# Optimization experiments

Hardware: AMD Instinct MI355X
Metric: run time of the kernel (lower is better)

Reference implementation:

```python
import jax, jax.numpy as jnp
import numpy as np

N, C, H, W = 16, 512, 64, 64
C_BAR, C_HAT = 64, 256


def max_pool2(t):
    # t: [n, c, h, w] -> [n, c, h//2, w//2] via 2x2 max pool
    n, c, h, w = t.shape
    return t.reshape(n, c, h // 2, 2, w // 2, 2).max(axis=(3, 5))


def setup_inputs() -> dict:
    key = jax.random.key(0)
    ks = jax.random.split(key, 6)
    x = jax.random.normal(ks[0], (N, C, H, W), dtype=jnp.float32)
    # 1x1 conv weights stored as [out_channels, in_channels]
    w_theta = jax.random.normal(ks[1], (C_BAR, C), dtype=jnp.float32) * 0.02
    w_phi = jax.random.normal(ks[2], (C_BAR, C), dtype=jnp.float32) * 0.02
    w_g = jax.random.normal(ks[3], (C_HAT, C), dtype=jnp.float32) * 0.02
    w_o = jax.random.normal(ks[4], (C, C_HAT), dtype=jnp.float32) * 0.02
    # gamma initialized to zero in the module; use a small nonzero value so the
    # attention path contributes to the output (and to gradients).
    gamma = jnp.full((1,), 0.1, dtype=jnp.float32)
    return {"x": x, "w_theta": w_theta, "w_phi": w_phi, "w_g": w_g,
            "w_o": w_o, "gamma": gamma}


def reference(x, w_theta, w_phi, w_g, w_o, gamma):
    n, c, h, w = x.shape
    hw, hw4 = h * w, (h * w) // 4
    # 1x1 conv projections (pure channel GEMMs)
    g_x = jnp.einsum('nchw,oc->nohw', x, w_g)          # [n, c_hat, h, w]
    g_x = max_pool2(g_x).reshape(n, -1, hw4)            # [n, c_hat, hw/4]
    phi_x = jnp.einsum('nchw,oc->nohw', x, w_phi)       # [n, c_bar, h, w]
    phi_x = max_pool2(phi_x).reshape(n, -1, hw4)        # [n, c_bar, hw/4]
    theta_x = jnp.einsum('nchw,oc->nohw', x, w_theta).reshape(n, -1, hw)  # [n, c_bar, hw]
    # bmm -> softmax -> bmm
    scores = jnp.einsum('nds,ndt->nst', theta_x, phi_x)  # [n, hw, hw/4]
    attn = jax.nn.softmax(scores, axis=-1)
    y = jnp.einsum('ndt,nst->nds', g_x, attn)            # [n, c_hat, hw]
    y = y.reshape(n, -1, h, w)
    o = jnp.einsum('nchw,oc->nohw', y, w_o)              # [n, c, h, w]
    return gamma[0] * o + x
```

## Files before the change

kernel.cpp:

```cpp
#include <hip/hip_runtime.h>
#include <stdint.h>

typedef unsigned short u16;
typedef u16   us4 __attribute__((ext_vector_type(4)));
typedef u16   us8 __attribute__((ext_vector_type(8)));
typedef __bf16 bf8 __attribute__((ext_vector_type(8)));
typedef float f4  __attribute__((ext_vector_type(4)));

__device__ __forceinline__ u16 f2bf(float f) {
    uint32_t u = __builtin_bit_cast(uint32_t, f);
    uint32_t r = (u + 0x7fffu + ((u >> 16) & 1u)) >> 16;
    return (u16)r;
}
__device__ __forceinline__ float bf2f(u16 s) {
    uint32_t u = ((uint32_t)s) << 16;
    return __builtin_bit_cast(float, u);
}
__device__ __forceinline__ f4 mfma16(bf8 a, bf8 b, f4 c) {
    return __builtin_amdgcn_mfma_f32_16x16x32_bf16(a, b, c, 0, 0, 0);
}
__device__ __forceinline__ u16 max4bf(u16 a, u16 b, u16 c, u16 d) {
    float m = fmaxf(fmaxf(bf2f(a), bf2f(b)), fmaxf(bf2f(c), bf2f(d)));
    return f2bf(m);
}

__global__ __launch_bounds__(256) void xt_kernel(
    const float* __restrict__ x, u16* __restrict__ Xt)
{
    const int s0 = blockIdx.x * 64, c0 = blockIdx.y * 64, n = blockIdx.z;
    const int tid = threadIdx.x;
    __shared__ u16 lds[64 * 72];

    {
        int c_loc = tid & 63, s_seg = (tid >> 6) * 16;
        const float* src = x + ((size_t)n * 512 + c0 + c_loc) * 4096 + s0 + s_seg;
        for (int i4 = 0; i4 < 4; i4++) {
            float4 f = *(const float4*)(src + i4 * 4);
            int s = s_seg + i4 * 4;
            lds[(s + 0) * 72 + c_loc] = f2bf(f.x);
            lds[(s + 1) * 72 + c_loc] = f2bf(f.y);
            lds[(s + 2) * 72 + c_loc] = f2bf(f.z);
            lds[(s + 3) * 72 + c_loc] = f2bf(f.w);
        }
    }
    __syncthreads();
    {
        int s_loc = tid >> 2, c_seg = (tid & 3) * 16;
        u16* dst = Xt + ((size_t)n * 4096 + s0 + s_loc) * 512 + c0 + c_seg;
        *(us8*)(dst)     = *(const us8*)&lds[s_loc * 72 + c_seg];
        *(us8*)(dst + 8) = *(const us8*)&lds[s_loc * 72 + c_seg + 8];
    }
}

__global__ __launch_bounds__(256) void wconv_kernel(
    const float* __restrict__ w_theta, const float* __restrict__ w_phi,
    const float* __restrict__ w_g, const float* __restrict__ w_o,
    u16* __restrict__ Wall_bf, u16* __restrict__ Wo_bf)
{
    int base = (blockIdx.x * 256 + threadIdx.x) * 4;
    const float* src; u16* dst;
    if (base < 32768)       { src = w_theta + base;          dst = Wall_bf + base; }
    else if (base < 65536)  { src = w_phi + (base - 32768);  dst = Wall_bf + base; }
    else if (base < 196608) { src = w_g + (base - 65536);    dst = Wall_bf + base; }
    else                    { src = w_o + (base - 196608);   dst = Wo_bf + (base - 196608); }
    float4 f = *(const float4*)src;
    us4 v; v[0] = f2bf(f.x); v[1] = f2bf(f.y); v[2] = f2bf(f.z); v[3] = f2bf(f.w);
    *(us4*)dst = v;
}

__global__ __launch_bounds__(256) void projT_gemm(
    const u16* __restrict__ Xt, const u16* __restrict__ Wall_bf,
    u16* __restrict__ PT)
{
    const int s0 = blockIdx.x * 128;
    const int r0 = blockIdx.y * 128;
    const int nb = blockIdx.z;
    const int tid = threadIdx.x;
    const int wave = tid >> 6, lane = tid & 63;
    const int quad = lane >> 4, l15 = lane & 15;
    const int wm = (wave >> 1) * 64, wn = (wave & 1) * 64;

    __shared__ u16 a_lds[128 * 40];
    __shared__ u16 b_lds[128 * 40];

    f4 acc[4][4];
    f4 z = {0.f, 0.f, 0.f, 0.f};
    for (int i = 0; i < 4; i++) for (int j = 0; j < 4; j++) acc[i][j] = z;

    const u16* Abase = Xt + ((size_t)nb * 4096 + s0) * 512;
    const int m = tid >> 1, kseg = (tid & 1) * 16;

    for (int k0 = 0; k0 < 512; k0 += 32) {
        *(us8*)&a_lds[m * 40 + kseg]     = *(const us8*)(Abase + (size_t)m * 512 + k0 + kseg);
        *(us8*)&a_lds[m * 40 + kseg + 8] = *(const us8*)(Abase + (size_t)m * 512 + k0 + kseg + 8);
        *(us8*)&b_lds[m * 40 + kseg]     = *(const us8*)(Wall_bf + (size_t)(r0 + m) * 512 + k0 + kseg);
        *(us8*)&b_lds[m * 40 + kseg + 8] = *(const us8*)(Wall_bf + (size_t)(r0 + m) * 512 + k0 + kseg + 8);
        __syncthreads();
        bf8 af[4], bfr[4];
        for (int i = 0; i < 4; i++)
            af[i]  = __builtin_bit_cast(bf8, *(const us8*)&a_lds[(wm + i*16 + l15)*40 + quad*8]);
        for (int j = 0; j < 4; j++)
            bfr[j] = __builtin_bit_cast(bf8, *(const us8*)&b_lds[(wn + j*16 + l15)*40 + quad*8]);
        for (int i = 0; i < 4; i++)
            for (int j = 0; j < 4; j++)
                acc[i][j] = mfma16(af[i], bfr[j], acc[i][j]);
        __syncthreads();
    }
    for (int i = 0; i < 4; i++) {
        int s_idx = s0 + wm + i * 16 + quad * 4;
        for (int rr = 0; rr < 4; rr++) {
            u16* dst = PT + ((size_t)nb * 4096 + s_idx + rr) * 384 + r0 + wn + l15;
            for (int j = 0; j < 4; j++)
                dst[j * 16] = f2bf(acc[i][j][rr]);
        }
    }
}

__global__ __launch_bounds__(256) void phi_pool2(
    const u16* __restrict__ PT, u16* __restrict__ phiT)
{
    int n = blockIdx.y, t0 = blockIdx.x * 64;
    int tid = threadIdx.x;
    int t_loc = tid >> 2, d0 = (tid & 3) * 16;
    int t = t0 + t_loc;
    int h2 = t >> 5, w2 = t & 31;
    int s00 = h2 * 128 + w2 * 2;
    const u16* base = PT + ((size_t)n * 4096) * 384 + 64 + d0;
    us8 r[4][2];
    int soff[4] = {s00, s00 + 1, s00 + 64, s00 + 65};
    for (int p = 0; p < 4; p++) {
        r[p][0] = *(const us8*)(base + (size_t)soff[p] * 384);
        r[p][1] = *(const us8*)(base + (size_t)soff[p] * 384 + 8);
    }
    us8 o0, o1;
    for (int i = 0; i < 8; i++) {
        o0[i] = max4bf(r[0][0][i], r[1][0][i], r[2][0][i], r[3][0][i]);
        o1[i] = max4bf(r[0][1][i], r[1][1][i], r[2][1][i], r[3][1][i]);
    }
    u16* dst = phiT + ((size_t)n * 1024 + t) * 64 + d0;
    *(us8*)dst = o0;
    *(us8*)(dst + 8) = o1;
}

__global__ __launch_bounds__(256) void g_poolT(
    const u16* __restrict__ PT, u16* __restrict__ gP)
{
    int t0 = blockIdx.x * 64, d0 = blockIdx.y * 64, n = blockIdx.z;
    int tid = threadIdx.x;
    __shared__ u16 lds[64 * 72];

    {
        int t_loc = tid & 63, dseg = (tid >> 6) * 16;
        int t = t0 + t_loc;
        int h2 = t >> 5, w2 = t & 31;
        int s00 = h2 * 128 + w2 * 2;
        const u16* base = PT + ((size_t)n * 4096) * 384 + 128 + d0 + dseg;
        us8 r[4][2];
        int soff[4] = {s00, s00 + 1, s00 + 64, s00 + 65};
        for (int p = 0; p < 4; p++) {
            r[p][0] = *(const us8*)(base + (size_t)soff[p] * 384);
            r[p][1] = *(const us8*)(base + (size_t)soff[p] * 384 + 8);
        }
        for (int i = 0; i < 8; i++) {
            lds[(dseg + i) * 72 + t_loc]     = max4bf(r[0][0][i], r[1][0][i], r[2][0][i], r[3][0][i]);
            lds[(dseg + 8 + i) * 72 + t_loc] = max4bf(r[0][1][i], r[1][1][i], r[2][1][i], r[3][1][i]);
        }
    }
    __syncthreads();
    {
        int d_loc = tid >> 2, t_seg = (tid & 3) * 16;
        u16* dst = gP + ((size_t)n * 256 + d0 + d_loc) * 1024 + t0 + t_seg;
        *(us8*)(dst)     = *(const us8*)&lds[d_loc * 72 + t_seg];
        *(us8*)(dst + 8) = *(const us8*)&lds[d_loc * 72 + t_seg + 8];
    }
}

__global__ __launch_bounds__(256) void attn_kernel(
    const u16* __restrict__ PT, const u16* __restrict__ phiT,
    const u16* __restrict__ gP, u16* __restrict__ yT)
{
    int n = blockIdx.y;
    int tid = threadIdx.x;
    int wave = tid >> 6, lane = tid & 63, quad = lane >> 4, l15 = lane & 15;
    int q0 = blockIdx.x * 64 + wave * 16;

    __shared__ u16 phi_lds[32 * 72];
    __shared__ u16 g_lds[256 * 40];
    __shared__ u16 p_lds[4][16 * 40];

    const u16* th = PT + ((size_t)n * 4096 + q0 + l15) * 384 + quad * 8;
    bf8 a0 = __builtin_bit_cast(bf8, *(const us8*)(th));
    bf8 a1 = __builtin_bit_cast(bf8, *(const us8*)(th + 32));

    f4 z = {0.f, 0.f, 0.f, 0.f};
    f4 acc[16];
    for (int b = 0; b < 16; b++) acc[b] = z;
    float lsum[4] = {0.f, 0.f, 0.f, 0.f};

    for (int tc = 0; tc < 1024; tc += 32) {
        {
            int t_loc = tid >> 3, d0 = (tid & 7) * 8;
            *(us8*)&phi_lds[t_loc * 72 + d0] =
                *(const us8*)(phiT + ((size_t)n * 1024 + tc + t_loc) * 64 + d0);
        }
        {
            const u16* src = gP + ((size_t)n * 256 + tid) * 1024 + tc;
            *(us8*)&g_lds[tid * 40 + 0]  = *(const us8*)(src);
            *(us8*)&g_lds[tid * 40 + 8]  = *(const us8*)(src + 8);
            *(us8*)&g_lds[tid * 40 + 16] = *(const us8*)(src + 16);
            *(us8*)&g_lds[tid * 40 + 24] = *(const us8*)(src + 24);
        }
        __syncthreads();

        for (int tt = 0; tt < 32; tt += 16) {
            bf8 b0 = __builtin_bit_cast(bf8, *(const us8*)&phi_lds[(tt + l15) * 72 + quad * 8]);
            bf8 b1 = __builtin_bit_cast(bf8, *(const us8*)&phi_lds[(tt + l15) * 72 + 32 + quad * 8]);
            f4 s = mfma16(a0, b0, z);
            s = mfma16(a1, b1, s);
            for (int rr = 0; rr < 4; rr++) {
                float p = __expf(s[rr]);
                lsum[rr] += p;
                p_lds[wave][(quad * 4 + rr) * 40 + tt + l15] = f2bf(p);
            }
        }
        bf8 ap = __builtin_bit_cast(bf8, *(const us8*)&p_lds[wave][l15 * 40 + quad * 8]);
        for (int b = 0; b < 16; b++) {
            bf8 bg = __builtin_bit_cast(bf8, *(const us8*)&g_lds[(b * 16 + l15) * 40 + quad * 8]);
            acc[b] = mfma16(ap, bg, acc[b]);
        }
        __syncthreads();
    }

    for (int rr = 0; rr < 4; rr++) {
        float v = lsum[rr];
        v += __shfl_xor(v, 1);
        v += __shfl_xor(v, 2);
        v += __shfl_xor(v, 4);
        v += __shfl_xor(v, 8);
        lsum[rr] = 1.0f / v;
    }
    for (int b = 0; b < 16; b++)
        for (int rr = 0; rr < 4; rr++) {
            size_t row = (size_t)n * 4096 + q0 + quad * 4 + rr;
            yT[row * 256 + b * 16 + l15] = f2bf(acc[b][rr] * lsum[rr]);
        }
}

__global__ __launch_bounds__(256) void oproj_gemm(
    const u16* __restrict__ Wo_bf, const u16* __restrict__ yT,
    const float* __restrict__ x, const float* __restrict__ gamma,
    float* __restrict__ out)
{
    const int nt = blockIdx.x;
    const int mt = blockIdx.y;
    const int nb = blockIdx.z;
    const int tid = threadIdx.x;
    const int wave = tid >> 6, lane = tid & 63;
    const int quad = lane >> 4, l15 = lane & 15;
    const int wm = (wave >> 1) * 32, wn = (wave & 1) * 64;
    const int s0 = nt * 128;

    __shared__ u16 a_lds[64 * 40];
    __shared__ u16 b_lds[128 * 40];

    f4 acc[2][4];
    f4 z = {0.f, 0.f, 0.f, 0.f};
    for (int i = 0; i < 2; i++) for (int j = 0; j < 4; j++) acc[i][j] = z;

    for (int k0 = 0; k0 < 256; k0 += 32) {
        {
            int m = tid >> 2, kq = (tid & 3) * 8;
            *(us8*)&a_lds[m * 40 + kq] =
                *(const us8*)(Wo_bf + (size_t)(mt * 64 + m) * 256 + k0 + kq);
        }
        {
            int s_loc = tid >> 1, kq = (tid & 1) * 16;
            const u16* src = yT + ((size_t)nb * 4096 + s0 + s_loc) * 256 + k0 + kq;
            *(us8*)&b_lds[s_loc * 40 + kq]     = *(const us8*)(src);
            *(us8*)&b_lds[s_loc * 40 + kq + 8] = *(const us8*)(src + 8);
        }
        __syncthreads();
        bf8 af[2], bfr[4];
        for (int i = 0; i < 2; i++)
            af[i] = __builtin_bit_cast(bf8, *(const us8*)&a_lds[(wm + i*16 + l15)*40 + quad*8]);
        for (int j = 0; j < 4; j++)
            bfr[j] = __builtin_bit_cast(bf8, *(const us8*)&b_lds[(wn + j*16 + l15)*40 + quad*8]);
        for (int i = 0; i < 2; i++)
            for (int j = 0; j < 4; j++)
                acc[i][j] = mfma16(af[i], bfr[j], acc[i][j]);
        __syncthreads();
    }
    float g0 = gamma[0];
    for (int i = 0; i < 2; i++) {
        int c = mt * 64 + wm + i * 16 + quad * 4;
        for (int j = 0; j < 4; j++) {
            int s = s0 + wn + j * 16 + l15;
            for (int rr = 0; rr < 4; rr++) {
                size_t idx = ((size_t)nb * 512 + c + rr) * 4096 + s;
                out[idx] = g0 * acc[i][j][rr] + x[idx];
            }
        }
    }
}

extern "C" void kernel_launch(void* const* d_in, const int* in_sizes, int n_in,
                              void* d_out, int out_size, void* d_ws, size_t ws_size,
                              hipStream_t stream)
{
    (void)in_sizes; (void)n_in; (void)out_size; (void)ws_size;
    const float* x       = (const float*)d_in[0];
    const float* w_theta = (const float*)d_in[1];
    const float* w_phi   = (const float*)d_in[2];
    const float* w_g     = (const float*)d_in[3];
    const float* w_o     = (const float*)d_in[4];
    const float* gamma   = (const float*)d_in[5];
    float* out = (float*)d_out;

    char* ws = (char*)d_ws;
    u16* Xt      = (u16*)(ws);
    u16* yT      = (u16*)(ws);
    u16* phiT    = (u16*)(ws + 33554432);
    u16* gP      = (u16*)(ws + 35651584);
    u16* Wall_bf = (u16*)(ws + 67108864);
    u16* Wo_bf   = (u16*)(ws + 67502080);
    u16* PT      = (u16*)(ws + 67764224);

    xt_kernel  <<<dim3(64, 8, 16), 256, 0, stream>>>(x, Xt);
    wconv_kernel<<<320, 256, 0, stream>>>(w_theta, w_phi, w_g, w_o, Wall_bf, Wo_bf);
    projT_gemm <<<dim3(32, 3, 16), 256, 0, stream>>>(Xt, Wall_bf, PT);
    phi_pool2  <<<dim3(16, 16),    256, 0, stream>>>(PT, phiT);
    g_poolT    <<<dim3(16, 4, 16), 256, 0, stream>>>(PT, gP);
    attn_kernel<<<dim3(64, 16),    256, 0, stream>>>(PT, phiT, gP, yT);
    oproj_gemm <<<dim3(32, 8, 16), 256, 0, stream>>>(Wo_bf, yT, x, gamma, out);
}
```

Before: 453.9 us.

## Register-prefetch next phi/g chunk and transpose MFMA operands for vectorized P and y stores

The attention kernel now loads the next 32-key chunk of phi and g into registers while the current chunk is computed, then writes it to LDS after a barrier. This hides global load latency behind the MFMA work. MFMA operand roles are swapped so each lane owns one query row, which turns the P writes to LDS and the final y stores into packed 4-element vector stores. The row-sum reduction shrinks to two cross-lane shuffles. The cost is an extra barrier per iteration and higher register pressure from the prefetch buffers.

```diff
diff --git a/kernel.cpp b/kernel.cpp
--- a/kernel.cpp
+++ b/kernel.cpp
@@ -189,61 +189,78 @@
     __shared__ u16 p_lds[4][16 * 40];
 
     const u16* th = PT + ((size_t)n * 4096 + q0 + l15) * 384 + quad * 8;
-    bf8 a0 = __builtin_bit_cast(bf8, *(const us8*)(th));
-    bf8 a1 = __builtin_bit_cast(bf8, *(const us8*)(th + 32));
+    bf8 bth0 = __builtin_bit_cast(bf8, *(const us8*)(th));
+    bf8 bth1 = __builtin_bit_cast(bf8, *(const us8*)(th + 32));
+
+    const int t_loc = tid >> 3, d0 = (tid & 7) * 8;
+    const u16* phi_src = phiT + ((size_t)n * 1024 + t_loc) * 64 + d0;
+    const u16* g_src   = gP + ((size_t)n * 256 + tid) * 1024;
 
     f4 z = {0.f, 0.f, 0.f, 0.f};
     f4 acc[16];
     for (int b = 0; b < 16; b++) acc[b] = z;
-    float lsum[4] = {0.f, 0.f, 0.f, 0.f};
-
-    for (int tc = 0; tc < 1024; tc += 32) {
-        {
-            int t_loc = tid >> 3, d0 = (tid & 7) * 8;
-            *(us8*)&phi_lds[t_loc * 72 + d0] =
-                *(const us8*)(phiT + ((size_t)n * 1024 + tc + t_loc) * 64 + d0);
-        }
-        {
-            const u16* src = gP + ((size_t)n * 256 + tid) * 1024 + tc;
-            *(us8*)&g_lds[tid * 40 + 0]  = *(const us8*)(src);
-            *(us8*)&g_lds[tid * 40 + 8]  = *(const us8*)(src + 8);
-            *(us8*)&g_lds[tid * 40 + 16] = *(const us8*)(src + 16);
-            *(us8*)&g_lds[tid * 40 + 24] = *(const us8*)(src + 24);
-        }
-        __syncthreads();
+    float lsum = 0.f;
+
+    us8 pf_phi = *(const us8*)(phi_src);
+    us8 pf_g0  = *(const us8*)(g_src + 0);
+    us8 pf_g1  = *(const us8*)(g_src + 8);
+    us8 pf_g2  = *(const us8*)(g_src + 16);
+    us8 pf_g3  = *(const us8*)(g_src + 24);
+    *(us8*)&phi_lds[t_loc * 72 + d0] = pf_phi;
+    *(us8*)&g_lds[tid * 40 + 0]  = pf_g0;
+    *(us8*)&g_lds[tid * 40 + 8]  = pf_g1;
+    *(us8*)&g_lds[tid * 40 + 16] = pf_g2;
+    *(us8*)&g_lds[tid * 40 + 24] = pf_g3;
+    __syncthreads();
+
+    for (int ci = 0; ci < 32; ci++) {
+        int nc = (ci + 1 < 32) ? (ci + 1) : ci;
+        pf_phi = *(const us8*)(phi_src + (size_t)nc * 2048);
+        pf_g0  = *(const us8*)(g_src + nc * 32 + 0);
+        pf_g1  = *(const us8*)(g_src + nc * 32 + 8);
+        pf_g2  = *(const us8*)(g_src + nc * 32 + 16);
+        pf_g3  = *(const us8*)(g_src + nc * 32 + 24);
 
         for (int tt = 0; tt < 32; tt += 16) {
-            bf8 b0 = __builtin_bit_cast(bf8, *(const us8*)&phi_lds[(tt + l15) * 72 + quad * 8]);
-            bf8 b1 = __builtin_bit_cast(bf8, *(const us8*)&phi_lds[(tt + l15) * 72 + 32 + quad * 8]);
-            f4 s = mfma16(a0, b0, z);
-            s = mfma16(a1, b1, s);
+            bf8 ap0 = __builtin_bit_cast(bf8, *(const us8*)&phi_lds[(tt + l15) * 72 + quad * 8]);
+            bf8 ap1 = __builtin_bit_cast(bf8, *(const us8*)&phi_lds[(tt + l15) * 72 + 32 + quad * 8]);
+            f4 s = mfma16(ap0, bth0, z);
+            s = mfma16(ap1, bth1, s);
+            us4 pk;
+            float ps = 0.f;
             for (int rr = 0; rr < 4; rr++) {
                 float p = __expf(s[rr]);
-                lsum[rr] += p;
-                p_lds[wave][(quad * 4 + rr) * 40 + tt + l15] = f2bf(p);
+                ps += p;
+                pk[rr] = f2bf(p);
             }
-        }
-        bf8 ap = __builtin_bit_cast(bf8, *(const us8*)&p_lds[wave][l15 * 40 + quad * 8]);
+            lsum += ps;
+            *(us4*)&p_lds[wave][l15 * 40 + tt + quad * 4] = pk;
+        }
+        bf8 bp = __builtin_bit_cast(bf8, *(const us8*)&p_lds[wave][l15 * 40 + quad * 8]);
         for (int b = 0; b < 16; b++) {
-            bf8 bg = __builtin_bit_cast(bf8, *(const us8*)&g_lds[(b * 16 + l15) * 40 + quad * 8]);
-            acc[b] = mfma16(ap, bg, acc[b]);
-        }
-        __syncthreads();
-    }
-
-    for (int rr = 0; rr < 4; rr++) {
-        float v = lsum[rr];
-        v += __shfl_xor(v, 1);
-        v += __shfl_xor(v, 2);
-        v += __shfl_xor(v, 4);
-        v += __shfl_xor(v, 8);
-        lsum[rr] = 1.0f / v;
-    }
-    for (int b = 0; b < 16; b++)
-        for (int rr = 0; rr < 4; rr++) {
-            size_t row = (size_t)n * 4096 + q0 + quad * 4 + rr;
-            yT[row * 256 + b * 16 + l15] = f2bf(acc[b][rr] * lsum[rr]);
-        }
+            bf8 ag = __builtin_bit_cast(bf8, *(const us8*)&g_lds[(b * 16 + l15) * 40 + quad * 8]);
+            acc[b] = mfma16(ag, bp, acc[b]);
+        }
+        __syncthreads();
+        *(us8*)&phi_lds[t_loc * 72 + d0] = pf_phi;
+        *(us8*)&g_lds[tid * 40 + 0]  = pf_g0;
+        *(us8*)&g_lds[tid * 40 + 8]  = pf_g1;
+        *(us8*)&g_lds[tid * 40 + 16] = pf_g2;
+        *(us8*)&g_lds[tid * 40 + 24] = pf_g3;
+        __syncthreads();
+    }
+
+    float v = lsum;
+    v += __shfl_xor(v, 16);
+    v += __shfl_xor(v, 32);
+    float inv = 1.0f / v;
+
+    u16* dst = yT + ((size_t)n * 4096 + q0 + l15) * 256 + quad * 4;
+    for (int b = 0; b < 16; b++) {
+        us4 o;
+        for (int rr = 0; rr < 4; rr++) o[rr] = f2bf(acc[b][rr] * inv);
+        *(us4*)(dst + b * 16) = o;
+    }
 }
 
 __global__ __launch_bounds__(256) void oproj_gemm(
```

After: 433.8 us. -4.4%, faster.
